# Performance work log

Measured on AMD Instinct MI355X. Metric: run time of the kernel, lower is better.

Reference implementation:

```python
import jax, jax.numpy as jnp
import numpy as np
from functools import partial

B = 256          # batch_size (== hidden_dim, required by the module's broadcasting)
T = 512          # seq_length
H = 256          # hidden_dim == dim_out
E = 6            # emb_dim
V = 10           # num_input_digits
C = 10           # num_classes


def _kaiming(key, shape):
    fan_in = shape[1]
    return jax.random.normal(key, shape, dtype=jnp.float32) * np.sqrt(2.0 / fan_in)


def setup_inputs() -> dict:
    key = jax.random.key(0)
    ks = jax.random.split(key, 12)
    inp = {
        "x": jax.random.randint(ks[0], (B, T), 0, V),
        "emb": jax.random.normal(ks[1], (V, E), dtype=jnp.float32),
        "Wxg": _kaiming(ks[2], (H, E)), "Whg": _kaiming(ks[3], (H, H)), "bg": jnp.zeros((H,), jnp.float32),
        "Wxi": _kaiming(ks[4], (H, E)), "Whi": _kaiming(ks[5], (H, H)), "bi": jnp.zeros((H,), jnp.float32),
        "Wxf": _kaiming(ks[6], (H, E)), "Whf": _kaiming(ks[7], (H, H)), "bf": jnp.zeros((H,), jnp.float32),
        "Wxo": _kaiming(ks[8], (H, E)), "Who": _kaiming(ks[9], (H, H)), "bo": jnp.zeros((H,), jnp.float32),
        "Wp": _kaiming(ks[10], (C, H)), "bp": jnp.zeros((C,), jnp.float32),
    }
    return inp


def reference(x, emb, Wxg, Whg, bg, Wxi, Whi, bi, Wxf, Whf, bf, Wxo, Who, bo, Wp, bp):
    # x: (B, T) int -> embed -> (B, T, E)
    xe = emb[x]
    # time-major (T, E, B): each step uses x_t.T as in the torch code
    xt_seq = jnp.transpose(xe, (1, 2, 0))

    h0 = jnp.zeros((H, B), jnp.float32)  # h lives as (H, B) per original math
    c0 = jnp.zeros((H, B), jnp.float32)

    def step(carry, xTt):  # xTt: (E, B)
        h, c = carry
        # NOTE: bias (H,) broadcasts over the trailing batch axis (H==B), faithful
        # to the original torch broadcasting.
        g = jnp.tanh(Wxg @ xTt + Whg @ h + bg)
        i = jax.nn.sigmoid(Wxi @ xTt + Whi @ h + bi)
        f = jax.nn.sigmoid(Wxf @ xTt + Whf @ h + bf)
        o = jax.nn.sigmoid(Wxo @ xTt + Who @ h + bo)
        c = g * i + c * f
        h = jnp.tanh(c) * o
        return (h, c), None

    (h, c), _ = jax.lax.scan(step, (h0, c0), xt_seq)
    return (Wp @ h).T + bp  # (B, C)
```

## Files before the change

### kernel.cpp

```cpp
#include <hip/hip_runtime.h>
#include <hip/hip_bf16.h>


typedef __attribute__((ext_vector_type(4))) int   int4v;
typedef __attribute__((ext_vector_type(4))) float float4v;

#define MFMA_I8(a, b, c) __builtin_amdgcn_mfma_i32_16x16x64_i8(a, b, c, 0, 0, 0)

#define K_TANH (-2.8853900817779268f)
#define K_SIG  (-1.4426950408889634f)

#define HSTRIDE 320

__device__ __forceinline__ short f2b(float f) {
    __hip_bfloat16 b = __float2bfloat16(f); return *(short*)&b;
}
__device__ __forceinline__ float b2f(short s) {
    union { unsigned int u; float f; } v; v.u = ((unsigned int)(unsigned short)s) << 16; return v.f;
}
__device__ __forceinline__ float fexp2(float x) {
#if __has_builtin(__builtin_amdgcn_exp2f)
    return __builtin_amdgcn_exp2f(x);
#else
    return __expf(x * 0.6931471805599453f);
#endif
}
__device__ __forceinline__ float frcp(float x) { return __builtin_amdgcn_rcpf(x); }

__global__ __attribute__((amdgpu_flat_work_group_size(512, 512), amdgpu_waves_per_eu(2, 2)))
void lstm_i8(
    const int* __restrict__ x,
    const float* __restrict__ emb,
    const float* __restrict__ Wxg, const float* __restrict__ Whg, const float* __restrict__ bg,
    const float* __restrict__ Wxi, const float* __restrict__ Whi, const float* __restrict__ bi,
    const float* __restrict__ Wxf, const float* __restrict__ Whf, const float* __restrict__ bff,
    const float* __restrict__ Wxo, const float* __restrict__ Who, const float* __restrict__ bo,
    const float* __restrict__ Wp, const float* __restrict__ bp,
    float* __restrict__ out)
{
    const int tid = threadIdx.x, bid = blockIdx.x;
    const int c0 = bid * 2;
    const int w = tid >> 6, lane = tid & 63;
    const int l = lane & 15, q = lane >> 4;
    const int col = lane & 1;
    const int rtb = (lane >> 1) & 1;
    const int si  = (lane >> 2) & 3;
    const int rwb = 32 * w;
    const int row = rwb + 16 * rtb + 4 * q + si;

    __shared__ __align__(16) unsigned int hbuf[2][2 * HSTRIDE / 4];
    __shared__ __align__(16) short hfin[2 * 264];
    __shared__ unsigned char xdig2[512 * 2];
    __shared__ __align__(16) float tblC[2 * 10 * 1024];
    __shared__ float scaleL[4 * 256];

    const float* WxT[4] = {Wxg, Wxi, Wxf, Wxo};
    const float* WhT[4] = {Whg, Whi, Whf, Who};
    const float* bT[4]  = {bg, bi, bff, bo};

    if (tid < 2 * HSTRIDE / 4) hbuf[0][tid] = 0u;
    for (int i = tid; i < 1024; i += 512)
        xdig2[i] = (unsigned char)x[(c0 + (i & 1)) * 512 + (i >> 1)];

    for (int i = tid; i < 5120; i += 512) {
        int cc  = i / 2560;
        int rem = i - cc * 2560;
        int d = rem >> 8, r = rem & 255;
        float4v v;
        #pragma unroll
        for (int g = 0; g < 4; g++) {
            float s = 0.f;
            #pragma unroll
            for (int e = 0; e < 6; e++) s += WxT[g][r * 6 + e] * emb[d * 6 + e];
            v[g] = (s + bT[g][c0 + cc]) * (g == 0 ? K_TANH : K_SIG);
        }
        *(float4v*)&tblC[cc * 10240 + d * 1024 + r * 4] = v;
    }

    int4v wa[2][4][4];
    #pragma unroll
    for (int rt = 0; rt < 2; rt++) {
        #pragma unroll
        for (int g = 0; g < 4; g++) {
            const float* Wr = WhT[g] + (rwb + rt * 16 + l) * 256 + q * 16;
            float mx = 0.f;
            #pragma unroll
            for (int kt = 0; kt < 4; kt++)
                #pragma unroll
                for (int c4 = 0; c4 < 4; c4++) {
                    float4v v = *(const float4v*)(Wr + kt * 64 + c4 * 4);
                    #pragma unroll
                    for (int j = 0; j < 4; j++) mx = fmaxf(mx, fabsf(v[j]));
                }
            mx = fmaxf(mx, __shfl_xor(mx, 16));
            mx = fmaxf(mx, __shfl_xor(mx, 32));
            mx = fmaxf(mx, 1e-20f);
            if (q == 0) scaleL[g * 256 + rwb + rt * 16 + l] = mx;
            float qs = 127.f / mx;
            #pragma unroll
            for (int kt = 0; kt < 4; kt++) {
                int4v f;
                #pragma unroll
                for (int dw = 0; dw < 4; dw++) {
                    float4v v = *(const float4v*)(Wr + kt * 64 + dw * 4);
                    int word = 0;
                    #pragma unroll
                    for (int byt = 0; byt < 4; byt++) {
                        int z = (int)rintf(v[byt] * qs);
                        word |= (z & 255) << (8 * byt);
                    }
                    f[dw] = word;
                }
                wa[rt][g][kt] = f;
            }
        }
    }

    __syncthreads();

    float dscl[4];
    #pragma unroll
    for (int g = 0; g < 4; g++) {
        float kk = (g == 0 ? K_TANH : K_SIG) * (1.f / 16129.f);
        dscl[g] = scaleL[g * 256 + row] * kk;
    }

    const bool bi1 = (si & 1) != 0;
    const bool bi2 = (si & 2) != 0;
    const bool brt = rtb != 0;
    const float* tprow = tblC + col * 10240 + row * 4;
    const int hoff = col * HSTRIDE + row;

    const int4v Z = {0, 0, 0, 0};

    float cs = 0.f, hl = 0.f;

    float4v tb;
    { int dg = xdig2[0 * 2 + col]; tb = *(const float4v*)(tprow + dg * 1024); }

    for (int t = 0; t < 512; t++) {
        const int p = t & 1;
        const char* hbase = (const char*)hbuf[p] + col * HSTRIDE + q * 16;

        int4v hf0 = *(const int4v*)(hbase + 0 * 64);
        int4v hf1 = *(const int4v*)(hbase + 1 * 64);
        int4v hf2 = *(const int4v*)(hbase + 2 * 64);
        int4v hf3 = *(const int4v*)(hbase + 3 * 64);

        int4v ag0 = MFMA_I8(wa[0][0][0], hf0, Z);
        int4v ag1 = MFMA_I8(wa[1][0][0], hf0, Z);
        int4v ai0 = MFMA_I8(wa[0][1][0], hf0, Z);
        int4v ai1 = MFMA_I8(wa[1][1][0], hf0, Z);
        int4v af0 = MFMA_I8(wa[0][2][0], hf0, Z);
        int4v af1 = MFMA_I8(wa[1][2][0], hf0, Z);
        int4v ao0 = MFMA_I8(wa[0][3][0], hf0, Z);
        int4v ao1 = MFMA_I8(wa[1][3][0], hf0, Z);
        ag0 = MFMA_I8(wa[0][0][1], hf1, ag0);
        ag1 = MFMA_I8(wa[1][0][1], hf1, ag1);
        ai0 = MFMA_I8(wa[0][1][1], hf1, ai0);
        ai1 = MFMA_I8(wa[1][1][1], hf1, ai1);
        af0 = MFMA_I8(wa[0][2][1], hf1, af0);
        af1 = MFMA_I8(wa[1][2][1], hf1, af1);
        ao0 = MFMA_I8(wa[0][3][1], hf1, ao0);
        ao1 = MFMA_I8(wa[1][3][1], hf1, ao1);
        ag0 = MFMA_I8(wa[0][0][2], hf2, ag0);
        ag1 = MFMA_I8(wa[1][0][2], hf2, ag1);
        ai0 = MFMA_I8(wa[0][1][2], hf2, ai0);
        ai1 = MFMA_I8(wa[1][1][2], hf2, ai1);
        af0 = MFMA_I8(wa[0][2][2], hf2, af0);
        af1 = MFMA_I8(wa[1][2][2], hf2, af1);
        ao0 = MFMA_I8(wa[0][3][2], hf2, ao0);
        ao1 = MFMA_I8(wa[1][3][2], hf2, ao1);

        float4v tbn;
        { int dgn = xdig2[((t + 1) & 511) * 2 + col]; tbn = *(const float4v*)(tprow + dgn * 1024); }

        ag0 = MFMA_I8(wa[0][0][3], hf3, ag0);
        ag1 = MFMA_I8(wa[1][0][3], hf3, ag1);
        int avg_;
        { int t0 = bi1 ? ag0[1] : ag0[0]; int t1 = bi1 ? ag0[3] : ag0[2]; int s0 = bi2 ? t1 : t0;
          int u0 = bi1 ? ag1[1] : ag1[0]; int u1 = bi1 ? ag1[3] : ag1[2]; int s1 = bi2 ? u1 : u0;
          avg_ = brt ? s1 : s0; }
        float pg = fmaf((float)avg_, dscl[0], tb[0]);
        float Eg = fexp2(pg);

        ai0 = MFMA_I8(wa[0][1][3], hf3, ai0);
        ai1 = MFMA_I8(wa[1][1][3], hf3, ai1);
        int avi_;
        { int t0 = bi1 ? ai0[1] : ai0[0]; int t1 = bi1 ? ai0[3] : ai0[2]; int s0 = bi2 ? t1 : t0;
          int u0 = bi1 ? ai1[1] : ai1[0]; int u1 = bi1 ? ai1[3] : ai1[2]; int s1 = bi2 ? u1 : u0;
          avi_ = brt ? s1 : s0; }
        float pi = fmaf((float)avi_, dscl[1], tb[1]);
        float Ei = fexp2(pi);
        float m1 = (1.f + Eg) * (1.f + Ei);

        af0 = MFMA_I8(wa[0][2][3], hf3, af0);
        af1 = MFMA_I8(wa[1][2][3], hf3, af1);
        int avf_;
        { int t0 = bi1 ? af0[1] : af0[0]; int t1 = bi1 ? af0[3] : af0[2]; int s0 = bi2 ? t1 : t0;
          int u0 = bi1 ? af1[1] : af1[0]; int u1 = bi1 ? af1[3] : af1[2]; int s1 = bi2 ? u1 : u0;
          avf_ = brt ? s1 : s0; }
        float pf = fmaf((float)avf_, dscl[2], tb[2]);
        float Ef = fexp2(pf);
        float fp1 = 1.f + Ef;
        float num = fmaf(cs, m1, (1.f - Eg) * fp1);
        float c   = num * frcp(m1 * fp1);
        cs = c;
        float Ec = fexp2(K_TANH * c);

        ao0 = MFMA_I8(wa[0][3][3], hf3, ao0);
        ao1 = MFMA_I8(wa[1][3][3], hf3, ao1);
        int avo_;
        { int t0 = bi1 ? ao0[1] : ao0[0]; int t1 = bi1 ? ao0[3] : ao0[2]; int s0 = bi2 ? t1 : t0;
          int u0 = bi1 ? ao1[1] : ao1[0]; int u1 = bi1 ? ao1[3] : ao1[2]; int s1 = bi2 ? u1 : u0;
          avo_ = brt ? s1 : s0; }
        float po = fmaf((float)avo_, dscl[3], tb[3]);
        float Eo = fexp2(po);
        float hh = (1.f - Ec) * frcp((1.f + Ec) * (1.f + Eo));
        hl = hh;
        *((char*)hbuf[1 - p] + hoff) = (char)((int)rintf(hh * 127.f));

        tb = tbn;
        __syncthreads();
    }

    hfin[col * 264 + row] = f2b(hl);
    __syncthreads();

    if (tid < 20) {
        int pc = tid / 10, cls = tid - pc * 10;
        const short* hcol = &hfin[pc * 264];
        const float* wrow = Wp + cls * 256;
        float s = 0.f;
        #pragma unroll 8
        for (int k = 0; k < 256; k++) s += b2f(hcol[k]) * wrow[k];
        out[(c0 + pc) * 10 + cls] = s + bp[cls];
    }
}

extern "C" void kernel_launch(void* const* d_in, const int* in_sizes, int n_in,
                              void* d_out, int out_size, void* d_ws, size_t ws_size,
                              hipStream_t stream) {
    const int*   x   = (const int*)d_in[0];
    const float* emb = (const float*)d_in[1];
    const float* Wxg = (const float*)d_in[2];
    const float* Whg = (const float*)d_in[3];
    const float* bg  = (const float*)d_in[4];
    const float* Wxi = (const float*)d_in[5];
    const float* Whi = (const float*)d_in[6];
    const float* bi  = (const float*)d_in[7];
    const float* Wxf = (const float*)d_in[8];
    const float* Whf = (const float*)d_in[9];
    const float* bff = (const float*)d_in[10];
    const float* Wxo = (const float*)d_in[11];
    const float* Who = (const float*)d_in[12];
    const float* bo  = (const float*)d_in[13];
    const float* Wp  = (const float*)d_in[14];
    const float* bp  = (const float*)d_in[15];

    hipLaunchKernelGGL(lstm_i8, dim3(128), dim3(512), 0, stream,
                       x, emb, Wxg, Whg, bg, Wxi, Whi, bi, Wxf, Whf, bff,
                       Wxo, Who, bo, Wp, bp, (float*)d_out);
}
```

Baseline: 544.2 us.

## Replace per-step block barrier with per-chunk LDS flag spin synchronization

Removes the __syncthreads at the end of every LSTM timestep. Instead, each wave pair bumps an LDS counter for the 64-row chunk of h it produced. Consumers spin on the four chunk flags and start each K-chunk's MFMAs as soon as that chunk is ready, reading chunks in an order rotated per pair and starting pairs staggered with s_nop. The aim is to let waves overlap instead of all stalling at a full barrier, at the cost of LDS polling traffic and a more fragile memory-ordering scheme that relies on relaxed atomics and lgkmcnt waits.

After: 615.8 us. 1.13x slower.

```diff
diff --git a/kernel.cpp b/kernel.cpp
--- a/kernel.cpp
+++ b/kernel.cpp
@@ -41,6 +41,7 @@
     const int tid = threadIdx.x, bid = blockIdx.x;
     const int c0 = bid * 2;
     const int w = tid >> 6, lane = tid & 63;
+    const int pair = w >> 1;
     const int l = lane & 15, q = lane >> 4;
     const int col = lane & 1;
     const int rtb = (lane >> 1) & 1;
@@ -53,12 +54,14 @@
     __shared__ unsigned char xdig2[512 * 2];
     __shared__ __align__(16) float tblC[2 * 10 * 1024];
     __shared__ float scaleL[4 * 256];
+    __shared__ __align__(16) int wflag[4];
 
     const float* WxT[4] = {Wxg, Wxi, Wxf, Wxo};
     const float* WhT[4] = {Whg, Whi, Whf, Who};
     const float* bT[4]  = {bg, bi, bff, bo};
 
     if (tid < 2 * HSTRIDE / 4) hbuf[0][tid] = 0u;
+    if (tid < 4) wflag[tid] = 0;
     for (int i = tid; i < 1024; i += 512)
         xdig2[i] = (unsigned char)x[(c0 + (i & 1)) * 512 + (i >> 1)];
 
@@ -98,7 +101,8 @@
             if (q == 0) scaleL[g * 256 + rwb + rt * 16 + l] = mx;
             float qs = 127.f / mx;
             #pragma unroll
-            for (int kt = 0; kt < 4; kt++) {
+            for (int c = 0; c < 4; c++) {
+                const int kt = (pair + c) & 3;
                 int4v f;
                 #pragma unroll
                 for (int dw = 0; dw < 4; dw++) {
@@ -111,7 +115,7 @@
                     }
                     f[dw] = word;
                 }
-                wa[rt][g][kt] = f;
+                wa[rt][g][c] = f;
             }
         }
     }
@@ -131,6 +135,13 @@
     const float* tprow = tblC + col * 10240 + row * 4;
     const int hoff = col * HSTRIDE + row;
 
+    const int kc0 = pair, kc1 = (pair + 1) & 3, kc2 = (pair + 2) & 3, kc3 = (pair + 3) & 3;
+    volatile int* vf0 = (volatile int*)&wflag[kc0];
+    volatile int* vf1 = (volatile int*)&wflag[kc1];
+    volatile int* vf2 = (volatile int*)&wflag[kc2];
+    volatile int* vf3 = (volatile int*)&wflag[kc3];
+    const int ho0 = kc0 * 64, ho1 = kc1 * 64, ho2 = kc2 * 64, ho3 = kc3 * 64;
+
     const int4v Z = {0, 0, 0, 0};
 
     float cs = 0.f, hl = 0.f;
@@ -138,45 +149,60 @@
     float4v tb;
     { int dg = xdig2[0 * 2 + col]; tb = *(const float4v*)(tprow + dg * 1024); }
 
+    for (int i = 0; i < pair * 50; i++) asm volatile("s_nop 7");
+
+    int f0 = 0, f1 = 0, f2 = 0, f3 = 0;
+
     for (int t = 0; t < 512; t++) {
         const int p = t & 1;
+        const int tgt = t << 1;
         const char* hbase = (const char*)hbuf[p] + col * HSTRIDE + q * 16;
 
-        int4v hf0 = *(const int4v*)(hbase + 0 * 64);
-        int4v hf1 = *(const int4v*)(hbase + 1 * 64);
-        int4v hf2 = *(const int4v*)(hbase + 2 * 64);
-        int4v hf3 = *(const int4v*)(hbase + 3 * 64);
-
-        int4v ag0 = MFMA_I8(wa[0][0][0], hf0, Z);
-        int4v ag1 = MFMA_I8(wa[1][0][0], hf0, Z);
-        int4v ai0 = MFMA_I8(wa[0][1][0], hf0, Z);
-        int4v ai1 = MFMA_I8(wa[1][1][0], hf0, Z);
-        int4v af0 = MFMA_I8(wa[0][2][0], hf0, Z);
-        int4v af1 = MFMA_I8(wa[1][2][0], hf0, Z);
-        int4v ao0 = MFMA_I8(wa[0][3][0], hf0, Z);
-        int4v ao1 = MFMA_I8(wa[1][3][0], hf0, Z);
-        ag0 = MFMA_I8(wa[0][0][1], hf1, ag0);
-        ag1 = MFMA_I8(wa[1][0][1], hf1, ag1);
-        ai0 = MFMA_I8(wa[0][1][1], hf1, ai0);
-        ai1 = MFMA_I8(wa[1][1][1], hf1, ai1);
-        af0 = MFMA_I8(wa[0][2][1], hf1, af0);
-        af1 = MFMA_I8(wa[1][2][1], hf1, af1);
-        ao0 = MFMA_I8(wa[0][3][1], hf1, ao0);
-        ao1 = MFMA_I8(wa[1][3][1], hf1, ao1);
-        ag0 = MFMA_I8(wa[0][0][2], hf2, ag0);
-        ag1 = MFMA_I8(wa[1][0][2], hf2, ag1);
-        ai0 = MFMA_I8(wa[0][1][2], hf2, ai0);
-        ai1 = MFMA_I8(wa[1][1][2], hf2, ai1);
-        af0 = MFMA_I8(wa[0][2][2], hf2, af0);
-        af1 = MFMA_I8(wa[1][2][2], hf2, af1);
-        ao0 = MFMA_I8(wa[0][3][2], hf2, ao0);
-        ao1 = MFMA_I8(wa[1][3][2], hf2, ao1);
+        if (f0 < tgt) { do { f0 = *vf0; } while (f0 < tgt); }
+        asm volatile("" ::: "memory");
+        int4v hfA = *(const int4v*)(hbase + ho0);
+        int4v ag0 = MFMA_I8(wa[0][0][0], hfA, Z);
+        int4v ag1 = MFMA_I8(wa[1][0][0], hfA, Z);
+        int4v ai0 = MFMA_I8(wa[0][1][0], hfA, Z);
+        int4v ai1 = MFMA_I8(wa[1][1][0], hfA, Z);
+        int4v af0 = MFMA_I8(wa[0][2][0], hfA, Z);
+        int4v af1 = MFMA_I8(wa[1][2][0], hfA, Z);
+        int4v ao0 = MFMA_I8(wa[0][3][0], hfA, Z);
+        int4v ao1 = MFMA_I8(wa[1][3][0], hfA, Z);
+
+        if (f1 < tgt) { do { f1 = *vf1; } while (f1 < tgt); }
+        asm volatile("" ::: "memory");
+        int4v hfB = *(const int4v*)(hbase + ho1);
+        ag0 = MFMA_I8(wa[0][0][1], hfB, ag0);
+        ag1 = MFMA_I8(wa[1][0][1], hfB, ag1);
+        ai0 = MFMA_I8(wa[0][1][1], hfB, ai0);
+        ai1 = MFMA_I8(wa[1][1][1], hfB, ai1);
+        af0 = MFMA_I8(wa[0][2][1], hfB, af0);
+        af1 = MFMA_I8(wa[1][2][1], hfB, af1);
+        ao0 = MFMA_I8(wa[0][3][1], hfB, ao0);
+        ao1 = MFMA_I8(wa[1][3][1], hfB, ao1);
+
+        if (f2 < tgt) { do { f2 = *vf2; } while (f2 < tgt); }
+        asm volatile("" ::: "memory");
+        int4v hfC = *(const int4v*)(hbase + ho2);
+        ag0 = MFMA_I8(wa[0][0][2], hfC, ag0);
+        ag1 = MFMA_I8(wa[1][0][2], hfC, ag1);
+        ai0 = MFMA_I8(wa[0][1][2], hfC, ai0);
+        ai1 = MFMA_I8(wa[1][1][2], hfC, ai1);
+        af0 = MFMA_I8(wa[0][2][2], hfC, af0);
+        af1 = MFMA_I8(wa[1][2][2], hfC, af1);
+        ao0 = MFMA_I8(wa[0][3][2], hfC, ao0);
+        ao1 = MFMA_I8(wa[1][3][2], hfC, ao1);
 
         float4v tbn;
         { int dgn = xdig2[((t + 1) & 511) * 2 + col]; tbn = *(const float4v*)(tprow + dgn * 1024); }
 
-        ag0 = MFMA_I8(wa[0][0][3], hf3, ag0);
-        ag1 = MFMA_I8(wa[1][0][3], hf3, ag1);
+        if (f3 < tgt) { do { f3 = *vf3; } while (f3 < tgt); }
+        asm volatile("" ::: "memory");
+        int4v hfD = *(const int4v*)(hbase + ho3);
+
+        ag0 = MFMA_I8(wa[0][0][3], hfD, ag0);
+        ag1 = MFMA_I8(wa[1][0][3], hfD, ag1);
         int avg_;
         { int t0 = bi1 ? ag0[1] : ag0[0]; int t1 = bi1 ? ag0[3] : ag0[2]; int s0 = bi2 ? t1 : t0;
           int u0 = bi1 ? ag1[1] : ag1[0]; int u1 = bi1 ? ag1[3] : ag1[2]; int s1 = bi2 ? u1 : u0;
@@ -184,8 +210,8 @@
         float pg = fmaf((float)avg_, dscl[0], tb[0]);
         float Eg = fexp2(pg);
 
-        ai0 = MFMA_I8(wa[0][1][3], hf3, ai0);
-        ai1 = MFMA_I8(wa[1][1][3], hf3, ai1);
+        ai0 = MFMA_I8(wa[0][1][3], hfD, ai0);
+        ai1 = MFMA_I8(wa[1][1][3], hfD, ai1);
         int avi_;
         { int t0 = bi1 ? ai0[1] : ai0[0]; int t1 = bi1 ? ai0[3] : ai0[2]; int s0 = bi2 ? t1 : t0;
           int u0 = bi1 ? ai1[1] : ai1[0]; int u1 = bi1 ? ai1[3] : ai1[2]; int s1 = bi2 ? u1 : u0;
@@ -194,8 +220,8 @@
         float Ei = fexp2(pi);
         float m1 = (1.f + Eg) * (1.f + Ei);
 
-        af0 = MFMA_I8(wa[0][2][3], hf3, af0);
-        af1 = MFMA_I8(wa[1][2][3], hf3, af1);
+        af0 = MFMA_I8(wa[0][2][3], hfD, af0);
+        af1 = MFMA_I8(wa[1][2][3], hfD, af1);
         int avf_;
         { int t0 = bi1 ? af0[1] : af0[0]; int t1 = bi1 ? af0[3] : af0[2]; int s0 = bi2 ? t1 : t0;
           int u0 = bi1 ? af1[1] : af1[0]; int u1 = bi1 ? af1[3] : af1[2]; int s1 = bi2 ? u1 : u0;
@@ -208,8 +234,8 @@
         cs = c;
         float Ec = fexp2(K_TANH * c);
 
-        ao0 = MFMA_I8(wa[0][3][3], hf3, ao0);
-        ao1 = MFMA_I8(wa[1][3][3], hf3, ao1);
+        ao0 = MFMA_I8(wa[0][3][3], hfD, ao0);
+        ao1 = MFMA_I8(wa[1][3][3], hfD, ao1);
         int avo_;
         { int t0 = bi1 ? ao0[1] : ao0[0]; int t1 = bi1 ? ao0[3] : ao0[2]; int s0 = bi2 ? t1 : t0;
           int u0 = bi1 ? ao1[1] : ao1[0]; int u1 = bi1 ? ao1[3] : ao1[2]; int s1 = bi2 ? u1 : u0;
@@ -218,11 +244,19 @@
         float Eo = fexp2(po);
         float hh = (1.f - Ec) * frcp((1.f + Ec) * (1.f + Eo));
         hl = hh;
+
         *((char*)hbuf[1 - p] + hoff) = (char)((int)rintf(hh * 127.f));
 
+        asm volatile("s_waitcnt lgkmcnt(0)" ::: "memory");
+        if (lane == 0)
+            __hip_atomic_fetch_add(&wflag[pair], 1, __ATOMIC_RELAXED, __HIP_MEMORY_SCOPE_WORKGROUP);
+
+        f0 = *vf0; f1 = *vf1; f2 = *vf2; f3 = *vf3;
+
         tb = tbn;
-        __syncthreads();
-    }
+    }
+
+    __syncthreads();
 
     hfin[col * 264 + row] = f2b(hl);
     __syncthreads();
```
